# Kernel optimization log

Hardware: AMD Instinct MI355X
Metric: run time of the kernel (lower is better)

## Reference

```python
import jax, jax.numpy as jnp
import numpy as np

EPS = 1e-12  # F.normalize default eps (denominator = max(norm, eps))


def setup_inputs() -> dict:
    key = jax.random.key(0)
    ks = jax.random.split(key, 8)
    B, FIN, H, W = 4, 256, 64, 64
    N_MEM, SQ = 64, 16           # sqrt_fin = fin**0.5
    POS_CH = 2                    # PosEncoding concatenates one coord channel per dim
    CIN = FIN + POS_CH
    QK = N_MEM * SQ               # 1024
    # PosEncoding buffer: normalized coordinate grid in [-1, 1], shape [2, H, W]
    ys = jnp.linspace(-1.0, 1.0, H, dtype=jnp.float32)
    xs = jnp.linspace(-1.0, 1.0, W, dtype=jnp.float32)
    gy, gx = jnp.meshgrid(ys, xs, indexing='ij')
    pos = jnp.stack([gy, gx], axis=0)
    s = 0.02
    return {
        'x':    jax.random.normal(ks[0], (B, FIN, H, W), jnp.float32),
        'pos':  pos,
        'wq':   jax.random.normal(ks[1], (QK, CIN), jnp.float32) * s,
        'bq':   jnp.zeros((QK,), jnp.float32),
        'wk':   jax.random.normal(ks[2], (QK, CIN), jnp.float32) * s,
        'bk':   jnp.zeros((QK,), jnp.float32),
        'v':    jax.random.normal(ks[3], (N_MEM, FIN), jnp.float32) * s,
        'wout': jax.random.normal(ks[4], (FIN, FIN), jnp.float32) * s,
        'bout': jnp.zeros((FIN,), jnp.float32),
    }


def reference(x, pos, wq, bq, wk, bk, v, wout, bout):
    B, C, H, W = x.shape
    S = H * W
    n_mem, fin = v.shape
    sq = wq.shape[0] // n_mem
    # PosEncoding: concat coordinate channels
    posb = jnp.broadcast_to(pos[None], (B,) + pos.shape)
    xp = jnp.concatenate([x, posb], axis=1).reshape(B, C + pos.shape[0], S)
    # 1x1 conv projections (channel GEMMs)
    q = jnp.einsum('oc,bcs->bos', wq, xp) + bq[None, :, None]  # [B, n_mem*sq, S]
    k = jnp.einsum('oc,bcs->bos', wk, xp) + bk[None, :, None]
    q = q.reshape(B, n_mem, sq, S).transpose(0, 3, 1, 2)  # [B,S,m,sq]
    k = k.reshape(B, n_mem, sq, S).transpose(0, 3, 2, 1)  # [B,S,sq,m]
    # F.normalize: q over last dim (sqrt_fin), k over dim=1 (sqrt_fin)
    qn = q / jnp.maximum(jnp.linalg.norm(q, axis=-1, keepdims=True), EPS)
    kn = k / jnp.maximum(jnp.linalg.norm(k, axis=2, keepdims=True), EPS)
    # attn[b,s,m,n] = qn . kn ; dropout is identity in eval mode.
    # mean over memory slots m commutes with (attn @ v), so fuse:
    attn_mean = jnp.einsum('bsk,bskn->bsn', qn.mean(axis=2), kn)  # [B,S,n_mem]
    mem = attn_mean @ v                                            # [B,S,fin]
    mem = mem.transpose(0, 2, 1).reshape(B, fin, H, W)
    out = jnp.einsum('of,bfhw->bohw', wout, mem) + bout[None, :, None, None]
    return x + out
```

## Files before the change

### kernel.cpp

```cpp
#include <hip/hip_runtime.h>
#include <stdint.h>

#define EPSN 1e-12f

typedef float f32x16 __attribute__((ext_vector_type(16)));
typedef float f32x4 __attribute__((ext_vector_type(4)));
typedef __bf16 bf16x8 __attribute__((ext_vector_type(8)));
typedef uint32_t u32x4 __attribute__((ext_vector_type(4)));

__device__ __forceinline__ unsigned short f2bf(float f) {
  union { float f; unsigned int u; } v; v.f = f;
  unsigned int u = v.u + 0x7FFFu + ((v.u >> 16) & 1u);
  return (unsigned short)(u >> 16);
}

#define WQF_OFF 0
#define WKF_OFF (32 * 18 * 64 * 8)
#define WVP_OFF (2 * 32 * 18 * 64 * 8)

__global__ __launch_bounds__(256) void prep_kernel(
    const float* __restrict__ wq, const float* __restrict__ bq,
    const float* __restrict__ wk, const float* __restrict__ bk,
    const float* __restrict__ v, const float* __restrict__ wout,
    unsigned short* __restrict__ wsp) {
  if (blockIdx.x < 144) {
    int t = blockIdx.x * 256 + threadIdx.x;
    int lane = t & 63;
    int rest = t >> 6;
    int ks = rest % 18, g = rest / 18;
    int o = g * 32 + (lane & 31);
    int kb = ks * 16 + (lane >> 5) * 8;
    unsigned short q8[8], k8[8];
#pragma unroll
    for (int j = 0; j < 8; ++j) {
      int k = kb + j;
      float vq, vk;
      if (k < 258)       { vq = wq[o * 258 + k]; vk = wk[o * 258 + k]; }
      else if (k == 258) { vq = bq[o];           vk = bk[o]; }
      else               { vq = 0.f;             vk = 0.f; }
      q8[j] = f2bf(vq); k8[j] = f2bf(vk);
    }
    *(u32x4*)(wsp + WQF_OFF + t * 8) = *(u32x4*)q8;
    *(u32x4*)(wsp + WKF_OFF + t * 8) = *(u32x4*)k8;
  } else {
    int idx2 = (blockIdx.x - 144) * 256 + threadIdx.x;
    int fc = idx2 & 3, m = (idx2 >> 2) & 63, o = idx2 >> 8;
    const f32x4* wo = (const f32x4*)(wout + o * 256 + fc * 64);
    const f32x4* vm = (const f32x4*)(v + m * 256 + fc * 64);
    float s = 0.f;
#pragma unroll
    for (int f = 0; f < 16; ++f) {
      f32x4 a = wo[f], bvv = vm[f];
      s += a[0]*bvv[0] + a[1]*bvv[1] + a[2]*bvv[2] + a[3]*bvv[3];
    }
    s += __shfl_xor(s, 1, 64);
    s += __shfl_xor(s, 2, 64);
    if (fc == 0) wsp[WVP_OFF + o * 64 + m] = f2bf(s);
  }
}

#define KP 296
#define QSS 33
#define AT 72

__global__ __launch_bounds__(1024, 8) void fused_kernel(
    const float* __restrict__ x, const float* __restrict__ pos,
    const unsigned short* __restrict__ wsp, const float* __restrict__ bout,
    float* __restrict__ out) {
  __shared__ __align__(16) unsigned short xp[32 * KP];
  __shared__ __align__(16) float qbarL[16 * QSS];
  __shared__ __align__(16) unsigned short attnM[32 * AT];
  __shared__ float boutL[256];

  const int tid = threadIdx.x;
  const int lane = tid & 63;
  const int wid = __builtin_amdgcn_readfirstlane(tid >> 6);
  const int px = lane & 31, q2 = lane >> 5;
  const int P0 = blockIdx.x * 32;
  const int b = P0 >> 12, s0 = P0 & 4095;

  uint32_t* xp32 = (uint32_t*)xp;
  for (int i = tid; i < 32 * 152; i += 1024) {
    int dc = i & 7, pp = (i >> 3) & 31, dh = i >> 8;
    int dcol = dh * 8 + dc;
    if (dcol < 148) {
      int c0 = dcol * 2;
      float v0, v1;
      if (c0 < 256) {
        v0 = x[(b * 256 + c0) * 4096 + s0 + pp];
        v1 = x[(b * 256 + c0 + 1) * 4096 + s0 + pp];
      } else if (c0 == 256) {
        v0 = pos[s0 + pp];
        v1 = pos[4096 + s0 + pp];
      } else {
        v0 = (c0 == 258) ? 1.0f : 0.0f;
        v1 = 0.0f;
      }
      xp32[pp * 148 + dcol] =
          (uint32_t)f2bf(v0) | ((uint32_t)f2bf(v1) << 16);
    }
  }
  if (tid < 256) boutL[tid] = bout[tid];
  if (tid < 16 * QSS) qbarL[tid] = 0.f;
  __syncthreads();

  const unsigned short* aqb = wsp + WQF_OFF + wid * 2 * 9216 + lane * 8;
  const unsigned short* akb = wsp + WKF_OFF + wid * 2 * 9216 + lane * 8;
  const unsigned short* xb = &xp[px * KP + q2 * 8];

  f32x16 acc0 = (f32x16)0.f, acc1 = (f32x16)0.f;
#pragma unroll
  for (int ks = 0; ks < 18; ++ks) {
    bf16x8 a0 = *(const bf16x8*)(aqb + ks * 512);
    bf16x8 a1 = *(const bf16x8*)(aqb + 9216 + ks * 512);
    bf16x8 bv = *(const bf16x8*)(xb + ks * 16);
    acc0 = __builtin_amdgcn_mfma_f32_32x32x16_bf16(a0, bv, acc0, 0, 0, 0);
    acc1 = __builtin_amdgcn_mfma_f32_32x32x16_bf16(a1, bv, acc1, 0, 0, 0);
  }

  {
    float qsum[8];
#pragma unroll
    for (int r = 0; r < 8; ++r) qsum[r] = 0.f;
#pragma unroll
    for (int t = 0; t < 2; ++t) {
      const f32x16 a = t ? acc1 : acc0;
      float s20 = 0.f, s21 = 0.f;
#pragma unroll
      for (int r = 0; r < 8; ++r) { s20 = fmaf(a[r], a[r], s20); s21 = fmaf(a[r + 8], a[r + 8], s21); }
      s20 += __shfl_xor(s20, 32, 64);
      s21 += __shfl_xor(s21, 32, 64);
      float i0 = 1.0f / fmaxf(sqrtf(s20), EPSN);
      float i1 = 1.0f / fmaxf(sqrtf(s21), EPSN);
#pragma unroll
      for (int r = 0; r < 8; ++r) qsum[r] += a[r] * i0 + a[r + 8] * i1;
    }
#pragma unroll
    for (int r = 0; r < 8; ++r) {
      int j = (r & 3) + ((r >> 2) << 3) + (q2 << 2);
      atomicAdd(&qbarL[j * QSS + px], qsum[r] * (1.0f / 64.0f));
    }
  }
  __syncthreads();

  acc0 = (f32x16)0.f; acc1 = (f32x16)0.f;
#pragma unroll
  for (int ks = 0; ks < 18; ++ks) {
    bf16x8 a0 = *(const bf16x8*)(akb + ks * 512);
    bf16x8 a1 = *(const bf16x8*)(akb + 9216 + ks * 512);
    bf16x8 bv = *(const bf16x8*)(xb + ks * 16);
    acc0 = __builtin_amdgcn_mfma_f32_32x32x16_bf16(a0, bv, acc0, 0, 0, 0);
    acc1 = __builtin_amdgcn_mfma_f32_32x32x16_bf16(a1, bv, acc1, 0, 0, 0);
  }

  {
    float qb[8];
#pragma unroll
    for (int r = 0; r < 8; ++r) {
      int j = (r & 3) + ((r >> 2) << 3) + (q2 << 2);
      qb[r] = qbarL[j * QSS + px];
    }
#pragma unroll
    for (int t = 0; t < 2; ++t) {
      const f32x16 a = t ? acc1 : acc0;
      float s20 = 0.f, s21 = 0.f, sp0 = 0.f, sp1 = 0.f;
#pragma unroll
      for (int r = 0; r < 8; ++r) {
        s20 = fmaf(a[r], a[r], s20);         sp0 = fmaf(qb[r], a[r], sp0);
        s21 = fmaf(a[r + 8], a[r + 8], s21); sp1 = fmaf(qb[r], a[r + 8], sp1);
      }
      s20 += __shfl_xor(s20, 32, 64);
      s21 += __shfl_xor(s21, 32, 64);
      sp0 += __shfl_xor(sp0, 32, 64);
      sp1 += __shfl_xor(sp1, 32, 64);
      if (q2 == 0) {
        int m0 = wid * 4 + t * 2;
        attnM[px * AT + m0]     = f2bf(sp0 / fmaxf(sqrtf(s20), EPSN));
        attnM[px * AT + m0 + 1] = f2bf(sp1 / fmaxf(sqrtf(s21), EPSN));
      }
    }
  }
  __syncthreads();

  if (wid < 8) {
    f32x16 e0 = (f32x16)0.f;
    const unsigned short* wv0 = wsp + WVP_OFF + (wid * 32 + px) * 64 + q2 * 8;
    const unsigned short* ab = &attnM[px * AT + q2 * 8];
#pragma unroll
    for (int ks = 0; ks < 4; ++ks) {
      bf16x8 a0 = *(const bf16x8*)(wv0 + ks * 16);
      bf16x8 bv = *(const bf16x8*)(ab + ks * 16);
      e0 = __builtin_amdgcn_mfma_f32_32x32x16_bf16(a0, bv, e0, 0, 0, 0);
    }
#pragma unroll
    for (int r = 0; r < 16; ++r) {
      const int o0 = wid * 32 + (r & 3) + (((r >> 2) & 1) << 3) + (q2 << 2) + ((r >> 3) << 4);
      const int gi0 = (b * 256 + o0) * 4096 + s0 + px;
      out[gi0] = x[gi0] + boutL[o0] + e0[r];
    }
  }
}

extern "C" void kernel_launch(void* const* d_in, const int* in_sizes, int n_in,
                              void* d_out, int out_size, void* d_ws, size_t ws_size,
                              hipStream_t stream) {
  const float* x    = (const float*)d_in[0];
  const float* pos  = (const float*)d_in[1];
  const float* wq   = (const float*)d_in[2];
  const float* bq   = (const float*)d_in[3];
  const float* wk   = (const float*)d_in[4];
  const float* bk   = (const float*)d_in[5];
  const float* v    = (const float*)d_in[6];
  const float* wout = (const float*)d_in[7];
  const float* bout = (const float*)d_in[8];
  float* out = (float*)d_out;
  unsigned short* wsp = (unsigned short*)d_ws;

  hipLaunchKernelGGL(prep_kernel, dim3(400), dim3(256), 0, stream,
                     wq, bq, wk, bk, v, wout, wsp);
  hipLaunchKernelGGL(fused_kernel, dim3(512), dim3(1024), 0, stream,
                     x, pos, wsp, bout, out);
}
```

Measured before the change: 136.4 us.

## Double pixel tile and stream projection weights through LDS with async DMA

Each block now processes 64 pixels instead of 32, so every weight fragment feeds two pixel sub-tiles and per-pixel weight traffic is halved. The Q/K weight fragments are brought in through a triple-buffered global-to-LDS DMA pipeline with explicit vmcnt waits, instead of direct global loads in the MFMA loop. The grid halves to 256 blocks and LDS use rises to about 140 KB, so occupancy drops to one block per CU. The prep kernel is also split so the Q and K weights are converted by separate threads.

```diff
diff --git a/kernel.cpp b/kernel.cpp
--- a/kernel.cpp
+++ b/kernel.cpp
@@ -12,6 +12,12 @@
   union { float f; unsigned int u; } v; v.f = f;
   unsigned int u = v.u + 0x7FFFu + ((v.u >> 16) & 1u);
   return (unsigned short)(u >> 16);
+}
+
+__device__ __forceinline__ void dma16(const void* g, void* l) {
+  __builtin_amdgcn_global_load_lds(
+      (const __attribute__((address_space(1))) unsigned int*)g,
+      (__attribute__((address_space(3))) unsigned int*)l, 16, 0, 0);
 }
 
 #define WQF_OFF 0
@@ -23,27 +29,30 @@
     const float* __restrict__ wk, const float* __restrict__ bk,
     const float* __restrict__ v, const float* __restrict__ wout,
     unsigned short* __restrict__ wsp) {
-  if (blockIdx.x < 144) {
-    int t = blockIdx.x * 256 + threadIdx.x;
-    int lane = t & 63;
-    int rest = t >> 6;
+  if (blockIdx.x < 288) {
+    int t2 = blockIdx.x * 256 + threadIdx.x;
+    int isK = t2 >= 36864;
+    int t = isK ? t2 - 36864 : t2;
+    const float* w = isK ? wk : wq;
+    const float* bb = isK ? bk : bq;
+    unsigned short* dst = wsp + (isK ? WKF_OFF : WQF_OFF);
+    int lane = t & 63, rest = t >> 6;
     int ks = rest % 18, g = rest / 18;
     int o = g * 32 + (lane & 31);
     int kb = ks * 16 + (lane >> 5) * 8;
-    unsigned short q8[8], k8[8];
+    unsigned short v8[8];
 #pragma unroll
     for (int j = 0; j < 8; ++j) {
       int k = kb + j;
-      float vq, vk;
-      if (k < 258)       { vq = wq[o * 258 + k]; vk = wk[o * 258 + k]; }
-      else if (k == 258) { vq = bq[o];           vk = bk[o]; }
-      else               { vq = 0.f;             vk = 0.f; }
-      q8[j] = f2bf(vq); k8[j] = f2bf(vk);
-    }
-    *(u32x4*)(wsp + WQF_OFF + t * 8) = *(u32x4*)q8;
-    *(u32x4*)(wsp + WKF_OFF + t * 8) = *(u32x4*)k8;
+      float val;
+      if (k < 258)       val = w[o * 258 + k];
+      else if (k == 258) val = bb[o];
+      else               val = 0.f;
+      v8[j] = f2bf(val);
+    }
+    *(u32x4*)(dst + t * 8) = *(u32x4*)v8;
   } else {
-    int idx2 = (blockIdx.x - 144) * 256 + threadIdx.x;
+    int idx2 = (blockIdx.x - 288) * 256 + threadIdx.x;
     int fc = idx2 & 3, m = (idx2 >> 2) & 63, o = idx2 >> 8;
     const f32x4* wo = (const f32x4*)(wout + o * 256 + fc * 64);
     const f32x4* vm = (const f32x4*)(v + m * 256 + fc * 64);
@@ -60,28 +69,29 @@
 }
 
 #define KP 296
-#define QSS 33
+#define QS 66
 #define AT 72
 
-__global__ __launch_bounds__(1024, 8) void fused_kernel(
+__global__ __launch_bounds__(1024, 4) void fused_kernel(
     const float* __restrict__ x, const float* __restrict__ pos,
     const unsigned short* __restrict__ wsp, const float* __restrict__ bout,
     float* __restrict__ out) {
-  __shared__ __align__(16) unsigned short xp[32 * KP];
-  __shared__ __align__(16) float qbarL[16 * QSS];
-  __shared__ __align__(16) unsigned short attnM[32 * AT];
+  __shared__ __align__(16) unsigned short aBuf[3 * 32 * 512];
+  __shared__ __align__(16) unsigned short xp[64 * KP];
+  __shared__ __align__(16) float qbarL[16 * QS];
+  __shared__ __align__(16) unsigned short attnM[64 * AT];
   __shared__ float boutL[256];
 
   const int tid = threadIdx.x;
   const int lane = tid & 63;
   const int wid = __builtin_amdgcn_readfirstlane(tid >> 6);
   const int px = lane & 31, q2 = lane >> 5;
-  const int P0 = blockIdx.x * 32;
+  const int P0 = blockIdx.x * 64;
   const int b = P0 >> 12, s0 = P0 & 4095;
 
   uint32_t* xp32 = (uint32_t*)xp;
-  for (int i = tid; i < 32 * 152; i += 1024) {
-    int dc = i & 7, pp = (i >> 3) & 31, dh = i >> 8;
+  for (int i = tid; i < 64 * 152; i += 1024) {
+    int dc = i & 7, pp = (i >> 3) & 63, dh = i >> 9;
     int dcol = dh * 8 + dc;
     if (dcol < 148) {
       int c0 = dcol * 2;
@@ -96,109 +106,147 @@
         v0 = (c0 == 258) ? 1.0f : 0.0f;
         v1 = 0.0f;
       }
-      xp32[pp * 148 + dcol] =
-          (uint32_t)f2bf(v0) | ((uint32_t)f2bf(v1) << 16);
+      xp32[pp * 148 + dcol] = (uint32_t)f2bf(v0) | ((uint32_t)f2bf(v1) << 16);
     }
   }
   if (tid < 256) boutL[tid] = bout[tid];
-  if (tid < 16 * QSS) qbarL[tid] = 0.f;
+  for (int i = tid; i < 16 * QS; i += 1024) qbarL[i] = 0.f;
   __syncthreads();
 
-  const unsigned short* aqb = wsp + WQF_OFF + wid * 2 * 9216 + lane * 8;
-  const unsigned short* akb = wsp + WKF_OFF + wid * 2 * 9216 + lane * 8;
-  const unsigned short* xb = &xp[px * KP + q2 * 8];
-
-  f32x16 acc0 = (f32x16)0.f, acc1 = (f32x16)0.f;
-#pragma unroll
-  for (int ks = 0; ks < 18; ++ks) {
-    bf16x8 a0 = *(const bf16x8*)(aqb + ks * 512);
-    bf16x8 a1 = *(const bf16x8*)(aqb + 9216 + ks * 512);
-    bf16x8 bv = *(const bf16x8*)(xb + ks * 16);
-    acc0 = __builtin_amdgcn_mfma_f32_32x32x16_bf16(a0, bv, acc0, 0, 0, 0);
-    acc1 = __builtin_amdgcn_mfma_f32_32x32x16_bf16(a1, bv, acc1, 0, 0, 0);
-  }
+#define ISSUE(wb, ks_) do {                                              \
+    int _sl = (ks_) % 3;                                                 \
+    dma16(wb + ((2 * wid) * 18 + (ks_)) * 512 + lane * 8,                \
+          &aBuf[_sl * 16384 + (2 * wid) * 512]);                         \
+    dma16(wb + ((2 * wid + 1) * 18 + (ks_)) * 512 + lane * 8,            \
+          &aBuf[_sl * 16384 + (2 * wid + 1) * 512]);                     \
+  } while (0)
+
+#define COMPUTE(ks_) do {                                                \
+    int _sl = (ks_) % 3;                                                 \
+    bf16x8 _a0 = *(const bf16x8*)&aBuf[_sl * 16384 + (2 * wid) * 512 + lane * 8];     \
+    bf16x8 _a1 = *(const bf16x8*)&aBuf[_sl * 16384 + (2 * wid + 1) * 512 + lane * 8]; \
+    bf16x8 _b0 = *(const bf16x8*)&xp[px * KP + (ks_) * 16 + q2 * 8];     \
+    bf16x8 _b1 = *(const bf16x8*)&xp[(32 + px) * KP + (ks_) * 16 + q2 * 8]; \
+    acc00 = __builtin_amdgcn_mfma_f32_32x32x16_bf16(_a0, _b0, acc00, 0, 0, 0); \
+    acc01 = __builtin_amdgcn_mfma_f32_32x32x16_bf16(_a0, _b1, acc01, 0, 0, 0); \
+    acc10 = __builtin_amdgcn_mfma_f32_32x32x16_bf16(_a1, _b0, acc10, 0, 0, 0); \
+    acc11 = __builtin_amdgcn_mfma_f32_32x32x16_bf16(_a1, _b1, acc11, 0, 0, 0); \
+  } while (0)
+
+#define PHASE(wb) do {                                                   \
+    ISSUE(wb, 0); ISSUE(wb, 1);                                          \
+    _Pragma("unroll 4")                                                  \
+    for (int ks = 0; ks < 16; ++ks) {                                    \
+      asm volatile("" ::: "memory");                                     \
+      ISSUE(wb, ks + 2);                                                 \
+      asm volatile("s_waitcnt vmcnt(4)" ::: "memory");                   \
+      COMPUTE(ks);                                                       \
+    }                                                                    \
+    asm volatile("s_waitcnt vmcnt(2)" ::: "memory");                     \
+    COMPUTE(16);                                                         \
+    asm volatile("s_waitcnt vmcnt(0)" ::: "memory");                     \
+    COMPUTE(17);                                                         \
+  } while (0)
+
+  f32x16 acc00 = (f32x16)0.f, acc01 = (f32x16)0.f,
+         acc10 = (f32x16)0.f, acc11 = (f32x16)0.f;
+  PHASE((wsp + WQF_OFF));
 
   {
-    float qsum[8];
-#pragma unroll
-    for (int r = 0; r < 8; ++r) qsum[r] = 0.f;
-#pragma unroll
-    for (int t = 0; t < 2; ++t) {
-      const f32x16 a = t ? acc1 : acc0;
-      float s20 = 0.f, s21 = 0.f;
-#pragma unroll
-      for (int r = 0; r < 8; ++r) { s20 = fmaf(a[r], a[r], s20); s21 = fmaf(a[r + 8], a[r + 8], s21); }
-      s20 += __shfl_xor(s20, 32, 64);
-      s21 += __shfl_xor(s21, 32, 64);
-      float i0 = 1.0f / fmaxf(sqrtf(s20), EPSN);
-      float i1 = 1.0f / fmaxf(sqrtf(s21), EPSN);
-#pragma unroll
-      for (int r = 0; r < 8; ++r) qsum[r] += a[r] * i0 + a[r + 8] * i1;
-    }
-#pragma unroll
-    for (int r = 0; r < 8; ++r) {
-      int j = (r & 3) + ((r >> 2) << 3) + (q2 << 2);
-      atomicAdd(&qbarL[j * QSS + px], qsum[r] * (1.0f / 64.0f));
-    }
+    float qsum[2][8];
+#pragma unroll
+    for (int nt = 0; nt < 2; ++nt)
+#pragma unroll
+      for (int r = 0; r < 8; ++r) qsum[nt][r] = 0.f;
+#pragma unroll
+    for (int ot = 0; ot < 2; ++ot) {
+#pragma unroll
+      for (int nt = 0; nt < 2; ++nt) {
+        const f32x16 a = ot ? (nt ? acc11 : acc10) : (nt ? acc01 : acc00);
+        float s20 = 0.f, s21 = 0.f;
+#pragma unroll
+        for (int r = 0; r < 8; ++r) {
+          s20 = fmaf(a[r], a[r], s20);
+          s21 = fmaf(a[r + 8], a[r + 8], s21);
+        }
+        s20 += __shfl_xor(s20, 32, 64);
+        s21 += __shfl_xor(s21, 32, 64);
+        float i0 = 1.0f / fmaxf(sqrtf(s20), EPSN);
+        float i1 = 1.0f / fmaxf(sqrtf(s21), EPSN);
+#pragma unroll
+        for (int r = 0; r < 8; ++r) qsum[nt][r] += a[r] * i0 + a[r + 8] * i1;
+      }
+    }
+#pragma unroll
+    for (int nt = 0; nt < 2; ++nt)
+#pragma unroll
+      for (int r = 0; r < 8; ++r) {
+        int j = (r & 3) + ((r >> 2) << 3) + (q2 << 2);
+        atomicAdd(&qbarL[j * QS + nt * 32 + px], qsum[nt][r] * (1.0f / 64.0f));
+      }
   }
   __syncthreads();
 
-  acc0 = (f32x16)0.f; acc1 = (f32x16)0.f;
-#pragma unroll
-  for (int ks = 0; ks < 18; ++ks) {
-    bf16x8 a0 = *(const bf16x8*)(akb + ks * 512);
-    bf16x8 a1 = *(const bf16x8*)(akb + 9216 + ks * 512);
-    bf16x8 bv = *(const bf16x8*)(xb + ks * 16);
-    acc0 = __builtin_amdgcn_mfma_f32_32x32x16_bf16(a0, bv, acc0, 0, 0, 0);
-    acc1 = __builtin_amdgcn_mfma_f32_32x32x16_bf16(a1, bv, acc1, 0, 0, 0);
-  }
+  acc00 = (f32x16)0.f; acc01 = (f32x16)0.f;
+  acc10 = (f32x16)0.f; acc11 = (f32x16)0.f;
+  PHASE((wsp + WKF_OFF));
 
   {
-    float qb[8];
-#pragma unroll
-    for (int r = 0; r < 8; ++r) {
-      int j = (r & 3) + ((r >> 2) << 3) + (q2 << 2);
-      qb[r] = qbarL[j * QSS + px];
-    }
-#pragma unroll
-    for (int t = 0; t < 2; ++t) {
-      const f32x16 a = t ? acc1 : acc0;
-      float s20 = 0.f, s21 = 0.f, sp0 = 0.f, sp1 = 0.f;
+    float qb[2][8];
+#pragma unroll
+    for (int nt = 0; nt < 2; ++nt)
 #pragma unroll
       for (int r = 0; r < 8; ++r) {
-        s20 = fmaf(a[r], a[r], s20);         sp0 = fmaf(qb[r], a[r], sp0);
-        s21 = fmaf(a[r + 8], a[r + 8], s21); sp1 = fmaf(qb[r], a[r + 8], sp1);
-      }
-      s20 += __shfl_xor(s20, 32, 64);
-      s21 += __shfl_xor(s21, 32, 64);
-      sp0 += __shfl_xor(sp0, 32, 64);
-      sp1 += __shfl_xor(sp1, 32, 64);
-      if (q2 == 0) {
-        int m0 = wid * 4 + t * 2;
-        attnM[px * AT + m0]     = f2bf(sp0 / fmaxf(sqrtf(s20), EPSN));
-        attnM[px * AT + m0 + 1] = f2bf(sp1 / fmaxf(sqrtf(s21), EPSN));
+        int j = (r & 3) + ((r >> 2) << 3) + (q2 << 2);
+        qb[nt][r] = qbarL[j * QS + nt * 32 + px];
+      }
+#pragma unroll
+    for (int ot = 0; ot < 2; ++ot) {
+#pragma unroll
+      for (int nt = 0; nt < 2; ++nt) {
+        const f32x16 a = ot ? (nt ? acc11 : acc10) : (nt ? acc01 : acc00);
+        float s20 = 0.f, s21 = 0.f, sp0 = 0.f, sp1 = 0.f;
+#pragma unroll
+        for (int r = 0; r < 8; ++r) {
+          s20 = fmaf(a[r], a[r], s20);         sp0 = fmaf(qb[nt][r], a[r], sp0);
+          s21 = fmaf(a[r + 8], a[r + 8], s21); sp1 = fmaf(qb[nt][r], a[r + 8], sp1);
+        }
+        s20 += __shfl_xor(s20, 32, 64);
+        s21 += __shfl_xor(s21, 32, 64);
+        sp0 += __shfl_xor(sp0, 32, 64);
+        sp1 += __shfl_xor(sp1, 32, 64);
+        if (q2 == 0) {
+          int m0 = wid * 4 + ot * 2;
+          attnM[(nt * 32 + px) * AT + m0]     = f2bf(sp0 / fmaxf(sqrtf(s20), EPSN));
+          attnM[(nt * 32 + px) * AT + m0 + 1] = f2bf(sp1 / fmaxf(sqrtf(s21), EPSN));
+        }
       }
     }
   }
   __syncthreads();
 
-  if (wid < 8) {
-    f32x16 e0 = (f32x16)0.f;
-    const unsigned short* wv0 = wsp + WVP_OFF + (wid * 32 + px) * 64 + q2 * 8;
-    const unsigned short* ab = &attnM[px * AT + q2 * 8];
+  {
+    const int otile = wid >> 1, pxt = wid & 1;
+    f32x16 e = (f32x16)0.f;
+    const unsigned short* wv = wsp + WVP_OFF + (otile * 32 + px) * 64 + q2 * 8;
+    const unsigned short* ab = &attnM[(pxt * 32 + px) * AT + q2 * 8];
 #pragma unroll
     for (int ks = 0; ks < 4; ++ks) {
-      bf16x8 a0 = *(const bf16x8*)(wv0 + ks * 16);
+      bf16x8 av = *(const bf16x8*)(wv + ks * 16);
       bf16x8 bv = *(const bf16x8*)(ab + ks * 16);
-      e0 = __builtin_amdgcn_mfma_f32_32x32x16_bf16(a0, bv, e0, 0, 0, 0);
+      e = __builtin_amdgcn_mfma_f32_32x32x16_bf16(av, bv, e, 0, 0, 0);
     }
 #pragma unroll
     for (int r = 0; r < 16; ++r) {
-      const int o0 = wid * 32 + (r & 3) + (((r >> 2) & 1) << 3) + (q2 << 2) + ((r >> 3) << 4);
-      const int gi0 = (b * 256 + o0) * 4096 + s0 + px;
-      out[gi0] = x[gi0] + boutL[o0] + e0[r];
-    }
-  }
+      const int o = otile * 32 + (r & 3) + ((r >> 2) << 3) + (q2 << 2);
+      const int p = pxt * 32 + px;
+      const int gi = (b * 256 + o) * 4096 + s0 + p;
+      out[gi] = x[gi] + boutL[o] + e[r];
+    }
+  }
+#undef PHASE
+#undef COMPUTE
+#undef ISSUE
 }
 
 extern "C" void kernel_launch(void* const* d_in, const int* in_sizes, int n_in,
@@ -216,8 +264,8 @@
   float* out = (float*)d_out;
   unsigned short* wsp = (unsigned short*)d_ws;
 
-  hipLaunchKernelGGL(prep_kernel, dim3(400), dim3(256), 0, stream,
+  hipLaunchKernelGGL(prep_kernel, dim3(544), dim3(256), 0, stream,
                      wq, bq, wk, bk, v, wout, wsp);
-  hipLaunchKernelGGL(fused_kernel, dim3(512), dim3(1024), 0, stream,
+  hipLaunchKernelGGL(fused_kernel, dim3(256), dim3(1024), 0, stream,
                      x, pos, wsp, bout, out);
 }
```

Result: no change. 136.3 us (-0.1%).

## Interleave Q and K projection GEMMs and retile weight prep and LDS layout

Applied to the files above, without the earlier changes.

Computes the Q and K projection MFMAs in a single k-loop that shares each LDS x fragment, rather than running two separate passes split by a barrier. The x tile in LDS moves to a fragment-major layout so each lane reads its 8 bf16 values contiguously. The prep kernel is rewritten to read weights row-wise with coalesced float2 loads and scatter them into the MFMA fragment layout, and the V·Wout product is split across more threads. Keeping four accumulators live raises register pressure, and the launch bound drops to 4 waves per EU, which may lower occupancy.

```diff
diff --git a/kernel.cpp b/kernel.cpp
--- a/kernel.cpp
+++ b/kernel.cpp
@@ -6,7 +6,6 @@
 typedef float f32x16 __attribute__((ext_vector_type(16)));
 typedef float f32x4 __attribute__((ext_vector_type(4)));
 typedef __bf16 bf16x8 __attribute__((ext_vector_type(8)));
-typedef uint32_t u32x4 __attribute__((ext_vector_type(4)));
 
 __device__ __forceinline__ unsigned short f2bf(float f) {
   union { float f; unsigned int u; } v; v.f = f;
@@ -23,51 +22,57 @@
     const float* __restrict__ wk, const float* __restrict__ bk,
     const float* __restrict__ v, const float* __restrict__ wout,
     unsigned short* __restrict__ wsp) {
-  if (blockIdx.x < 144) {
-    int t = blockIdx.x * 256 + threadIdx.x;
-    int lane = t & 63;
-    int rest = t >> 6;
-    int ks = rest % 18, g = rest / 18;
-    int o = g * 32 + (lane & 31);
-    int kb = ks * 16 + (lane >> 5) * 8;
-    unsigned short q8[8], k8[8];
-#pragma unroll
-    for (int j = 0; j < 8; ++j) {
-      int k = kb + j;
-      float vq, vk;
-      if (k < 258)       { vq = wq[o * 258 + k]; vk = wk[o * 258 + k]; }
-      else if (k == 258) { vq = bq[o];           vk = bk[o]; }
-      else               { vq = 0.f;             vk = 0.f; }
-      q8[j] = f2bf(vq); k8[j] = f2bf(vk);
-    }
-    *(u32x4*)(wsp + WQF_OFF + t * 8) = *(u32x4*)q8;
-    *(u32x4*)(wsp + WKF_OFF + t * 8) = *(u32x4*)k8;
+  int bid = blockIdx.x;
+  if (bid < 512) {
+    int isK = bid >= 256;
+    int ob = (bid & 255) * 4;
+    const float* w = isK ? wk : wq;
+    const float* bb = isK ? bk : bq;
+    unsigned short* dst = wsp + (isK ? WKF_OFF : WQF_OFF);
+    for (int i = threadIdx.x; i < 4 * 129; i += 256) {
+      int r = i / 129, q = i - r * 129;
+      int o = ob + r, k = q * 2;
+      float2 w2 = *(const float2*)(w + o * 258 + k);
+      int g = o >> 5, col = o & 31;
+      int ks = k >> 4, hi = (k >> 3) & 1, j = k & 7;
+      uint32_t pk = (uint32_t)f2bf(w2.x) | ((uint32_t)f2bf(w2.y) << 16);
+      *(uint32_t*)(dst + (((g * 18 + ks) * 64 + hi * 32 + col) << 3) + j) = pk;
+    }
+    for (int i = threadIdx.x; i < 4 * 30; i += 256) {
+      int r = i / 30, kk = 258 + (i - r * 30);
+      int o = ob + r;
+      int g = o >> 5, col = o & 31;
+      int ks = kk >> 4, hi = (kk >> 3) & 1, j = kk & 7;
+      dst[(((g * 18 + ks) * 64 + hi * 32 + col) << 3) + j] =
+          (kk == 258) ? f2bf(bb[o]) : (unsigned short)0;
+    }
   } else {
-    int idx2 = (blockIdx.x - 144) * 256 + threadIdx.x;
-    int fc = idx2 & 3, m = (idx2 >> 2) & 63, o = idx2 >> 8;
-    const f32x4* wo = (const f32x4*)(wout + o * 256 + fc * 64);
-    const f32x4* vm = (const f32x4*)(v + m * 256 + fc * 64);
+    int idx = (bid - 512) * 256 + threadIdx.x;
+    int fc = idx & 15, m = (idx >> 4) & 63, o = idx >> 10;
+    const f32x4* wo = (const f32x4*)(wout + o * 256 + fc * 16);
+    const f32x4* vm = (const f32x4*)(v + m * 256 + fc * 16);
     float s = 0.f;
 #pragma unroll
-    for (int f = 0; f < 16; ++f) {
+    for (int f = 0; f < 4; ++f) {
       f32x4 a = wo[f], bvv = vm[f];
       s += a[0]*bvv[0] + a[1]*bvv[1] + a[2]*bvv[2] + a[3]*bvv[3];
     }
     s += __shfl_xor(s, 1, 64);
     s += __shfl_xor(s, 2, 64);
+    s += __shfl_xor(s, 4, 64);
+    s += __shfl_xor(s, 8, 64);
     if (fc == 0) wsp[WVP_OFF + o * 64 + m] = f2bf(s);
   }
 }
 
-#define KP 296
 #define QSS 33
 #define AT 72
 
-__global__ __launch_bounds__(1024, 8) void fused_kernel(
+__global__ __launch_bounds__(1024, 4) void fused_kernel(
     const float* __restrict__ x, const float* __restrict__ pos,
     const unsigned short* __restrict__ wsp, const float* __restrict__ bout,
     float* __restrict__ out) {
-  __shared__ __align__(16) unsigned short xp[32 * KP];
+  __shared__ __align__(16) unsigned short xpF[18 * 2 * 32 * 8];
   __shared__ __align__(16) float qbarL[16 * QSS];
   __shared__ __align__(16) unsigned short attnM[32 * AT];
   __shared__ float boutL[256];
@@ -79,43 +84,44 @@
   const int P0 = blockIdx.x * 32;
   const int b = P0 >> 12, s0 = P0 & 4095;
 
-  uint32_t* xp32 = (uint32_t*)xp;
-  for (int i = tid; i < 32 * 152; i += 1024) {
-    int dc = i & 7, pp = (i >> 3) & 31, dh = i >> 8;
-    int dcol = dh * 8 + dc;
-    if (dcol < 148) {
-      int c0 = dcol * 2;
-      float v0, v1;
-      if (c0 < 256) {
-        v0 = x[(b * 256 + c0) * 4096 + s0 + pp];
-        v1 = x[(b * 256 + c0 + 1) * 4096 + s0 + pp];
-      } else if (c0 == 256) {
-        v0 = pos[s0 + pp];
-        v1 = pos[4096 + s0 + pp];
-      } else {
-        v0 = (c0 == 258) ? 1.0f : 0.0f;
-        v1 = 0.0f;
-      }
-      xp32[pp * 148 + dcol] =
-          (uint32_t)f2bf(v0) | ((uint32_t)f2bf(v1) << 16);
-    }
+  uint32_t* xp32 = (uint32_t*)xpF;
+  for (int i = tid; i < 32 * 144; i += 1024) {
+    int p = i & 31, dcol = i >> 5;
+    int c0 = dcol * 2;
+    float v0, v1;
+    if (c0 < 256) {
+      v0 = x[(b * 256 + c0) * 4096 + s0 + p];
+      v1 = x[(b * 256 + c0 + 1) * 4096 + s0 + p];
+    } else if (c0 == 256) {
+      v0 = pos[s0 + p];
+      v1 = pos[4096 + s0 + p];
+    } else {
+      v0 = (c0 == 258) ? 1.0f : 0.0f;
+      v1 = 0.0f;
+    }
+    xp32[(dcol >> 2) * 128 + p * 4 + (dcol & 3)] =
+        (uint32_t)f2bf(v0) | ((uint32_t)f2bf(v1) << 16);
   }
   if (tid < 256) boutL[tid] = bout[tid];
   if (tid < 16 * QSS) qbarL[tid] = 0.f;
   __syncthreads();
 
-  const unsigned short* aqb = wsp + WQF_OFF + wid * 2 * 9216 + lane * 8;
-  const unsigned short* akb = wsp + WKF_OFF + wid * 2 * 9216 + lane * 8;
-  const unsigned short* xb = &xp[px * KP + q2 * 8];
-
-  f32x16 acc0 = (f32x16)0.f, acc1 = (f32x16)0.f;
-#pragma unroll
+  const unsigned short* aq = wsp + WQF_OFF + (2 * wid) * 18 * 512 + lane * 8;
+  const unsigned short* ak = wsp + WKF_OFF + (2 * wid) * 18 * 512 + lane * 8;
+
+  f32x16 accq0 = (f32x16)0.f, accq1 = (f32x16)0.f,
+         acck0 = (f32x16)0.f, acck1 = (f32x16)0.f;
+#pragma unroll 3
   for (int ks = 0; ks < 18; ++ks) {
-    bf16x8 a0 = *(const bf16x8*)(aqb + ks * 512);
-    bf16x8 a1 = *(const bf16x8*)(aqb + 9216 + ks * 512);
-    bf16x8 bv = *(const bf16x8*)(xb + ks * 16);
-    acc0 = __builtin_amdgcn_mfma_f32_32x32x16_bf16(a0, bv, acc0, 0, 0, 0);
-    acc1 = __builtin_amdgcn_mfma_f32_32x32x16_bf16(a1, bv, acc1, 0, 0, 0);
+    bf16x8 bv = *(const bf16x8*)&xpF[(ks * 2 + q2) * 256 + px * 8];
+    bf16x8 aq0 = *(const bf16x8*)(aq + ks * 512);
+    bf16x8 aq1 = *(const bf16x8*)(aq + 9216 + ks * 512);
+    bf16x8 ak0 = *(const bf16x8*)(ak + ks * 512);
+    bf16x8 ak1 = *(const bf16x8*)(ak + 9216 + ks * 512);
+    accq0 = __builtin_amdgcn_mfma_f32_32x32x16_bf16(aq0, bv, accq0, 0, 0, 0);
+    accq1 = __builtin_amdgcn_mfma_f32_32x32x16_bf16(aq1, bv, accq1, 0, 0, 0);
+    acck0 = __builtin_amdgcn_mfma_f32_32x32x16_bf16(ak0, bv, acck0, 0, 0, 0);
+    acck1 = __builtin_amdgcn_mfma_f32_32x32x16_bf16(ak1, bv, acck1, 0, 0, 0);
   }
 
   {
@@ -124,10 +130,13 @@
     for (int r = 0; r < 8; ++r) qsum[r] = 0.f;
 #pragma unroll
     for (int t = 0; t < 2; ++t) {
-      const f32x16 a = t ? acc1 : acc0;
+      const f32x16 a = t ? accq1 : accq0;
       float s20 = 0.f, s21 = 0.f;
 #pragma unroll
-      for (int r = 0; r < 8; ++r) { s20 = fmaf(a[r], a[r], s20); s21 = fmaf(a[r + 8], a[r + 8], s21); }
+      for (int r = 0; r < 8; ++r) {
+        s20 = fmaf(a[r], a[r], s20);
+        s21 = fmaf(a[r + 8], a[r + 8], s21);
+      }
       s20 += __shfl_xor(s20, 32, 64);
       s21 += __shfl_xor(s21, 32, 64);
       float i0 = 1.0f / fmaxf(sqrtf(s20), EPSN);
@@ -143,16 +152,6 @@
   }
   __syncthreads();
 
-  acc0 = (f32x16)0.f; acc1 = (f32x16)0.f;
-#pragma unroll
-  for (int ks = 0; ks < 18; ++ks) {
-    bf16x8 a0 = *(const bf16x8*)(akb + ks * 512);
-    bf16x8 a1 = *(const bf16x8*)(akb + 9216 + ks * 512);
-    bf16x8 bv = *(const bf16x8*)(xb + ks * 16);
-    acc0 = __builtin_amdgcn_mfma_f32_32x32x16_bf16(a0, bv, acc0, 0, 0, 0);
-    acc1 = __builtin_amdgcn_mfma_f32_32x32x16_bf16(a1, bv, acc1, 0, 0, 0);
-  }
-
   {
     float qb[8];
 #pragma unroll
@@ -162,7 +161,7 @@
     }
 #pragma unroll
     for (int t = 0; t < 2; ++t) {
-      const f32x16 a = t ? acc1 : acc0;
+      const f32x16 a = t ? acck1 : acck0;
       float s20 = 0.f, s21 = 0.f, sp0 = 0.f, sp1 = 0.f;
 #pragma unroll
       for (int r = 0; r < 8; ++r) {
@@ -183,20 +182,20 @@
   __syncthreads();
 
   if (wid < 8) {
-    f32x16 e0 = (f32x16)0.f;
-    const unsigned short* wv0 = wsp + WVP_OFF + (wid * 32 + px) * 64 + q2 * 8;
+    f32x16 e = (f32x16)0.f;
+    const unsigned short* wv = wsp + WVP_OFF + (wid * 32 + px) * 64 + q2 * 8;
     const unsigned short* ab = &attnM[px * AT + q2 * 8];
 #pragma unroll
     for (int ks = 0; ks < 4; ++ks) {
-      bf16x8 a0 = *(const bf16x8*)(wv0 + ks * 16);
+      bf16x8 av = *(const bf16x8*)(wv + ks * 16);
       bf16x8 bv = *(const bf16x8*)(ab + ks * 16);
-      e0 = __builtin_amdgcn_mfma_f32_32x32x16_bf16(a0, bv, e0, 0, 0, 0);
+      e = __builtin_amdgcn_mfma_f32_32x32x16_bf16(av, bv, e, 0, 0, 0);
     }
 #pragma unroll
     for (int r = 0; r < 16; ++r) {
-      const int o0 = wid * 32 + (r & 3) + (((r >> 2) & 1) << 3) + (q2 << 2) + ((r >> 3) << 4);
-      const int gi0 = (b * 256 + o0) * 4096 + s0 + px;
-      out[gi0] = x[gi0] + boutL[o0] + e0[r];
+      const int o = wid * 32 + (r & 3) + (((r >> 2) & 1) << 3) + (q2 << 2) + ((r >> 3) << 4);
+      const int gi = (b * 256 + o) * 4096 + s0 + px;
+      out[gi] = x[gi] + boutL[o] + e[r];
     }
   }
 }
@@ -216,7 +215,7 @@
   float* out = (float*)d_out;
   unsigned short* wsp = (unsigned short*)d_ws;
 
-  hipLaunchKernelGGL(prep_kernel, dim3(400), dim3(256), 0, stream,
+  hipLaunchKernelGGL(prep_kernel, dim3(1536), dim3(256), 0, stream,
                      wq, bq, wk, bk, v, wout, wsp);
   hipLaunchKernelGGL(fused_kernel, dim3(512), dim3(1024), 0, stream,
                      x, pos, wsp, bout, out);
```

Result: slower. 140.9 us (+3.3%).
